# Performance work log

Hardware: AMD Instinct MI355X
Metric: run time of the kernel (lower is better)

Reference implementation:

```python
import jax, jax.numpy as jnp
import numpy as np

B, N, IN_F, OUT_F, H, NUM_EDGE_TYPES = 16, 512, 256, 256, 8, 50
HEAD_DIM = OUT_F // H
LN_EPS = 1e-5


def setup_inputs() -> dict:
    key = jax.random.key(0)
    ks = jax.random.split(key, 8)
    x = jax.random.normal(ks[0], (B, N, IN_F), dtype=jnp.float32)
    adj = jax.random.randint(ks[1], (B, N, N), 0, 2, dtype=jnp.int32)
    edge_types = jax.random.randint(ks[2], (B, N, N), 0, NUM_EDGE_TYPES, dtype=jnp.int32)
    # Parameters (torch Linear stores weight as [out, in]; we keep [in, out] for x @ W)
    W = jax.random.normal(ks[3], (IN_F, OUT_F), dtype=jnp.float32) / np.sqrt(IN_F)
    a1 = jax.random.normal(ks[4], (HEAD_DIM,), dtype=jnp.float32) / np.sqrt(HEAD_DIM)
    a2 = jax.random.normal(ks[5], (HEAD_DIM,), dtype=jnp.float32) / np.sqrt(HEAD_DIM)
    edge_emb = jax.random.normal(ks[6], (NUM_EDGE_TYPES, H), dtype=jnp.float32) * 0.02
    edge_emb = edge_emb.at[0].set(0.0)  # padding_idx=0
    ln_gamma = jnp.ones((OUT_F,), dtype=jnp.float32)
    ln_beta = jnp.zeros((OUT_F,), dtype=jnp.float32)
    return {"x": x, "adj": adj, "edge_types": edge_types, "W": W, "a1": a1,
            "a2": a2, "edge_emb": edge_emb, "ln_gamma": ln_gamma, "ln_beta": ln_beta}


def reference(x, adj, edge_types, W, a1, a2, edge_emb, ln_gamma, ln_beta):
    Bx, Nx, _ = x.shape
    # Wh: [B, N, H, D]
    Wh = (x @ W).reshape(Bx, Nx, H, HEAD_DIM)
    # per-node attention scalars: [B, N, H]
    s1 = jnp.einsum('bnhd,d->bnh', Wh, a1)
    s2 = jnp.einsum('bnhd,d->bnh', Wh, a2)
    # e: [B, N(i), N(j), H]
    e = s1[:, :, None, :] + s2[:, None, :, :] + edge_emb[edge_types]
    e = jnp.where(e > 0, e, 0.2 * e)  # leaky_relu(0.2)
    e = jnp.where((adj == 0)[..., None], jnp.float32(-1e9), e)
    alpha = jax.nn.softmax(e, axis=2)  # softmax over j
    # (dropout omitted: eval mode / deterministic reference)
    h = jnp.einsum('bijh,bjhd->bihd', alpha, Wh).reshape(Bx, Nx, OUT_F)
    # LayerNorm over last dim
    mu = jnp.mean(h, axis=-1, keepdims=True)
    var = jnp.mean(jnp.square(h - mu), axis=-1, keepdims=True)
    hn = (h - mu) * jax.lax.rsqrt(var + LN_EPS) * ln_gamma + ln_beta
    return jax.nn.elu(hn)
```

## Files before the change

### kernel.cpp

```cpp
#include <hip/hip_runtime.h>
#include <hip/hip_bf16.h>
#include <stdint.h>

namespace gat {
constexpr int NB   = 16;
constexpr int NN   = 512;
constexpr int FIN  = 256;
constexpr int FOUT = 256;
constexpr int H    = 8;
constexpr int NE   = 50;
constexpr float L2E  = 1.4426950408889634f;
constexpr float MASK = -115.41500f;
}
using namespace gat;

typedef __attribute__((ext_vector_type(8))) short short8;
typedef __attribute__((ext_vector_type(4))) float f32x4;

__device__ __forceinline__ unsigned pk_bf16(unsigned ulo, unsigned uhi) {
  return __builtin_amdgcn_perm(uhi, ulo, 0x07060302u);
}
__device__ __forceinline__ unsigned pk2f(float a, float b) {
  return pk_bf16(__float_as_uint(a) + 0x8000u, __float_as_uint(b) + 0x8000u);
}

__global__ __launch_bounds__(256) void k_prep(const float* __restrict__ Wm,
                                              unsigned short* __restrict__ WbT) {
  const int k  = threadIdx.x;
  const int f0 = blockIdx.x * 4;
  #pragma unroll
  for (int r = 0; r < 4; ++r) {
    const unsigned u = __float_as_uint(Wm[k * FOUT + f0 + r]) + 0x8000u;
    WbT[(f0 + r) * FIN + k] = (unsigned short)(u >> 16);
  }
}

__global__ __launch_bounds__(256, 4) void k_gemm(
    const float* __restrict__ x, const unsigned short* __restrict__ WbT,
    const float* __restrict__ a1, const float* __restrict__ a2,
    unsigned short* __restrict__ WhT, float* __restrict__ s1, float* __restrict__ s2T)
{
  __shared__ alignas(16) unsigned short xS[16 * 264];
  const int t    = threadIdx.x;
  const int row0 = blockIdx.x * 16;

  {
    const int r  = t >> 4;
    const int kb = (t & 15) * 16;
    const float4* xg = (const float4*)(x + (size_t)(row0 + r) * FIN + kb);
    const float4 v0 = xg[0], v1 = xg[1], v2 = xg[2], v3 = xg[3];
    uint4 o0, o1;
    o0.x = pk2f(v0.x, v0.y); o0.y = pk2f(v0.z, v0.w);
    o0.z = pk2f(v1.x, v1.y); o0.w = pk2f(v1.z, v1.w);
    o1.x = pk2f(v2.x, v2.y); o1.y = pk2f(v2.z, v2.w);
    o1.z = pk2f(v3.x, v3.y); o1.w = pk2f(v3.z, v3.w);
    *(uint4*)&xS[r * 264 + kb]     = o0;
    *(uint4*)&xS[r * 264 + kb + 8] = o1;
  }
  __syncthreads();

  const int w    = t >> 6;
  const int L    = t & 63;
  const int nn   = L & 15;
  const int quad = L >> 4;
  const unsigned short* wb = WbT + (size_t)(w * 64 + nn) * FIN + quad * 8;
  const unsigned short* xp = &xS[nn * 264 + quad * 8];

  f32x4 acc0 = {0.f,0.f,0.f,0.f}, acc1 = {0.f,0.f,0.f,0.f};
  f32x4 acc2 = {0.f,0.f,0.f,0.f}, acc3 = {0.f,0.f,0.f,0.f};

  #pragma unroll 2
  for (int kc = 0; kc < 8; ++kc) {
    const int k0 = kc * 32;
    const short8 A  = *(const short8*)(xp + k0);
    const short8 B0 = *(const short8*)(wb + k0);
    const short8 B1 = *(const short8*)(wb + 16 * FIN + k0);
    const short8 B2 = *(const short8*)(wb + 32 * FIN + k0);
    const short8 B3 = *(const short8*)(wb + 48 * FIN + k0);
    acc0 = __builtin_amdgcn_mfma_f32_16x16x32_bf16(A, B0, acc0, 0, 0, 0);
    acc1 = __builtin_amdgcn_mfma_f32_16x16x32_bf16(A, B1, acc1, 0, 0, 0);
    acc2 = __builtin_amdgcn_mfma_f32_16x16x32_bf16(A, B2, acc2, 0, 0, 0);
    acc3 = __builtin_amdgcn_mfma_f32_16x16x32_bf16(A, B3, acc3, 0, 0, 0);
  }

  const int b     = row0 >> 9;
  const int node0 = (row0 & 511) + quad * 4;
  f32x4 accs[4] = {acc0, acc1, acc2, acc3};

  #pragma unroll
  for (int ft = 0; ft < 4; ++ft) {
    const int f = w * 64 + ft * 16 + nn;
    uint2 o;
    o.x = pk2f(accs[ft][0], accs[ft][1]);
    o.y = pk2f(accs[ft][2], accs[ft][3]);
    *(uint2*)(WhT + (size_t)((b * 8 + (f >> 5)) * 32 + (f & 31)) * 512 + node0) = o;
  }

  const float a1lo = a1[nn], a1hi = a1[16 + nn];
  const float a2lo = a2[nn], a2hi = a2[16 + nn];
  #pragma unroll
  for (int hh = 0; hh < 2; ++hh) {
    const int h = w * 2 + hh;
    const f32x4 e0 = accs[hh * 2], e1 = accs[hh * 2 + 1];
    float p1[4], p2[4];
    #pragma unroll
    for (int r = 0; r < 4; ++r) {
      p1[r] = e0[r] * a1lo + e1[r] * a1hi;
      p2[r] = e0[r] * a2lo + e1[r] * a2hi;
    }
    #pragma unroll
    for (int r = 0; r < 4; ++r) {
      p1[r] += __shfl_xor(p1[r], 1); p2[r] += __shfl_xor(p2[r], 1);
      p1[r] += __shfl_xor(p1[r], 2); p2[r] += __shfl_xor(p2[r], 2);
      p1[r] += __shfl_xor(p1[r], 4); p2[r] += __shfl_xor(p2[r], 4);
      p1[r] += __shfl_xor(p1[r], 8); p2[r] += __shfl_xor(p2[r], 8);
    }
    if (nn == 0) {
      float4 sv; sv.x = p2[0] * L2E; sv.y = p2[1] * L2E; sv.z = p2[2] * L2E; sv.w = p2[3] * L2E;
      *(float4*)(s2T + (size_t)(b * 8 + h) * 512 + node0) = sv;
      #pragma unroll
      for (int r = 0; r < 4; ++r)
        s1[(size_t)(row0 + quad * 4 + r) * H + h] = p1[r] * L2E;
    }
  }
}

__global__ __launch_bounds__(256, 2) void k_attn(
    const int* __restrict__ adj, const int* __restrict__ ety,
    const float* __restrict__ s1, const float* __restrict__ s2T,
    const unsigned short* __restrict__ WhT, const float* __restrict__ emb,
    const float* __restrict__ gam, const float* __restrict__ bet,
    float* __restrict__ out)
{
  __shared__ float2 embS[4 * 64];
  __shared__ float2 lnS[16 * 4];

  const int t    = threadIdx.x;
  const int b    = blockIdx.x >> 5;
  const int i0   = (blockIdx.x & 31) * 16;
  const int w    = t >> 6;
  const int L    = t & 63;
  const int i    = L & 15;
  const int quad = L >> 4;
  const int h0   = w, h1 = w + 4;

  {
    const int wp = t >> 6, e = t & 63;
    if (e < NE) {
      float2 v; v.x = emb[e * H + wp] * L2E; v.y = emb[e * H + wp + 4] * L2E;
      embS[t] = v;
    }
  }

  const int row = b * NN + i0 + i;
  const float si0 = s1[(size_t)row * H + h0];
  const float si1 = s1[(size_t)row * H + h1];
  const int adjBase = row * NN;
  const float* s2h0 = s2T + (size_t)(b * 8 + h0) * 512;
  const float* s2h1 = s2T + (size_t)(b * 8 + h1) * 512;
  const unsigned short* wt00 = WhT + (size_t)((b * 8 + h0) * 32 + i)      * 512;
  const unsigned short* wt01 = WhT + (size_t)((b * 8 + h0) * 32 + 16 + i) * 512;
  const unsigned short* wt10 = WhT + (size_t)((b * 8 + h1) * 32 + i)      * 512;
  const unsigned short* wt11 = WhT + (size_t)((b * 8 + h1) * 32 + 16 + i) * 512;

  f32x4 acc00 = {0.f,0.f,0.f,0.f}, acc01 = {0.f,0.f,0.f,0.f};
  f32x4 acc10 = {0.f,0.f,0.f,0.f}, acc11 = {0.f,0.f,0.f,0.f};
  float l0 = 0.f, l1 = 0.f;

  __syncthreads();

  #pragma unroll 2
  for (int kc = 0; kc < 16; ++kc) {
    const int ja = kc * 32 + quad * 8;
    const int4 av0 = *(const int4*)(adj + adjBase + ja);
    const int4 av1 = *(const int4*)(adj + adjBase + ja + 4);
    const int4 ev0 = *(const int4*)(ety + adjBase + ja);
    const int4 ev1 = *(const int4*)(ety + adjBase + ja + 4);
    const float4 sa0 = *(const float4*)(s2h0 + ja);
    const float4 sb0 = *(const float4*)(s2h0 + ja + 4);
    const float4 sa1 = *(const float4*)(s2h1 + ja);
    const float4 sb1 = *(const float4*)(s2h1 + ja + 4);
    const short8 A00 = *(const short8*)(wt00 + ja);
    const short8 A01 = *(const short8*)(wt01 + ja);
    const short8 A10 = *(const short8*)(wt10 + ja);
    const short8 A11 = *(const short8*)(wt11 + ja);

    const int aq[8] = {av0.x, av0.y, av0.z, av0.w, av1.x, av1.y, av1.z, av1.w};
    const int eq[8] = {ev0.x, ev0.y, ev0.z, ev0.w, ev1.x, ev1.y, ev1.z, ev1.w};
    const float s20[8] = {sa0.x, sa0.y, sa0.z, sa0.w, sb0.x, sb0.y, sb0.z, sb0.w};
    const float s21[8] = {sa1.x, sa1.y, sa1.z, sa1.w, sb1.x, sb1.y, sb1.z, sb1.w};

    unsigned u0[8], u1[8];
    #pragma unroll
    for (int q = 0; q < 8; ++q) {
      const float2 em = embS[w * 64 + eq[q]];
      const bool on = (aq[q] != 0);
      float e0 = si0 + s20[q] + em.x;
      float e1 = si1 + s21[q] + em.y;
      e0 = fmaxf(e0, 0.2f * e0);
      e1 = fmaxf(e1, 0.2f * e1);
      e0 = on ? e0 : MASK;
      e1 = on ? e1 : MASK;
      const float p0 = exp2f(e0);
      const float p1 = exp2f(e1);
      l0 += p0; l1 += p1;
      u0[q] = __float_as_uint(p0) + 0x8000u;
      u1[q] = __float_as_uint(p1) + 0x8000u;
    }
    uint4 U0, U1;
    U0.x = pk_bf16(u0[0], u0[1]); U0.y = pk_bf16(u0[2], u0[3]);
    U0.z = pk_bf16(u0[4], u0[5]); U0.w = pk_bf16(u0[6], u0[7]);
    U1.x = pk_bf16(u1[0], u1[1]); U1.y = pk_bf16(u1[2], u1[3]);
    U1.z = pk_bf16(u1[4], u1[5]); U1.w = pk_bf16(u1[6], u1[7]);
    const short8 B0 = __builtin_bit_cast(short8, U0);
    const short8 B1 = __builtin_bit_cast(short8, U1);

    acc00 = __builtin_amdgcn_mfma_f32_16x16x32_bf16(A00, B0, acc00, 0, 0, 0);
    acc01 = __builtin_amdgcn_mfma_f32_16x16x32_bf16(A01, B0, acc01, 0, 0, 0);
    acc10 = __builtin_amdgcn_mfma_f32_16x16x32_bf16(A10, B1, acc10, 0, 0, 0);
    acc11 = __builtin_amdgcn_mfma_f32_16x16x32_bf16(A11, B1, acc11, 0, 0, 0);
  }

  l0 += __shfl_xor(l0, 16); l0 += __shfl_xor(l0, 32);
  l1 += __shfl_xor(l1, 16); l1 += __shfl_xor(l1, 32);
  const float inv0 = __builtin_amdgcn_rcpf(l0);
  const float inv1 = __builtin_amdgcn_rcpf(l1);

  float vals[16];
  #pragma unroll
  for (int r = 0; r < 4; ++r) {
    vals[r]      = acc00[r] * inv0;
    vals[4 + r]  = acc01[r] * inv0;
    vals[8 + r]  = acc10[r] * inv1;
    vals[12 + r] = acc11[r] * inv1;
  }

  float s = 0.f, ss = 0.f;
  #pragma unroll
  for (int k = 0; k < 16; ++k) { s += vals[k]; ss += vals[k] * vals[k]; }
  s += __shfl_xor(s, 16); ss += __shfl_xor(ss, 16);
  s += __shfl_xor(s, 32); ss += __shfl_xor(ss, 32);
  if (quad == 0) { float2 v; v.x = s; v.y = ss; lnS[i * 4 + w] = v; }
  __syncthreads();
  float S = 0.f, SS = 0.f;
  #pragma unroll
  for (int ww = 0; ww < 4; ++ww) { const float2 v = lnS[i * 4 + ww]; S += v.x; SS += v.y; }
  const float mu   = S * (1.0f / 256.0f);
  const float var  = SS * (1.0f / 256.0f) - mu * mu;
  const float rstd = rsqrtf(var + 1e-5f);

  const int fb[4] = { h0 * 32 + quad * 4, h0 * 32 + 16 + quad * 4,
                      h1 * 32 + quad * 4, h1 * 32 + 16 + quad * 4 };
  #pragma unroll
  for (int g = 0; g < 4; ++g) {
    const float4 gv = *(const float4*)(gam + fb[g]);
    const float4 bv = *(const float4*)(bet + fb[g]);
    float4 o;
    o.x = (vals[g*4+0] - mu) * rstd * gv.x + bv.x;
    o.y = (vals[g*4+1] - mu) * rstd * gv.y + bv.y;
    o.z = (vals[g*4+2] - mu) * rstd * gv.z + bv.z;
    o.w = (vals[g*4+3] - mu) * rstd * gv.w + bv.w;
    o.x = o.x > 0.f ? o.x : exp2f(o.x * L2E) - 1.f;
    o.y = o.y > 0.f ? o.y : exp2f(o.y * L2E) - 1.f;
    o.z = o.z > 0.f ? o.z : exp2f(o.z * L2E) - 1.f;
    o.w = o.w > 0.f ? o.w : exp2f(o.w * L2E) - 1.f;
    *(float4*)(out + (size_t)row * FOUT + fb[g]) = o;
  }
}

extern "C" void kernel_launch(void* const* d_in, const int* in_sizes, int n_in,
                              void* d_out, int out_size, void* d_ws, size_t ws_size,
                              hipStream_t stream) {
  (void)in_sizes; (void)n_in; (void)out_size; (void)ws_size;
  const float* x   = (const float*)d_in[0];
  const int*   adj = (const int*)  d_in[1];
  const int*   ety = (const int*)  d_in[2];
  const float* Wm  = (const float*)d_in[3];
  const float* a1  = (const float*)d_in[4];
  const float* a2  = (const float*)d_in[5];
  const float* emb = (const float*)d_in[6];
  const float* gam = (const float*)d_in[7];
  const float* bet = (const float*)d_in[8];
  float* out = (float*)d_out;

  unsigned short* WhT = (unsigned short*)d_ws;
  unsigned short* WbT = WhT + (size_t)NB * H * 32 * 512;
  float* s1  = (float*)(WbT + (size_t)FOUT * FIN);
  float* s2T = s1 + (size_t)NB * NN * H;

  k_prep<<<dim3(64),  dim3(256), 0, stream>>>(Wm, WbT);
  k_gemm<<<dim3(NB * NN / 16), dim3(256), 0, stream>>>(x, WbT, a1, a2, WhT, s1, s2T);
  k_attn<<<dim3(NB * (NN / 16)), dim3(256), 0, stream>>>(adj, ety, s1, s2T, WhT, emb, gam, bet, out);
}
```

Baseline: 141.5 us.

## Split K/J reduction across two wave groups with LDS combine in gemm and attention

Both the projection GEMM and the attention kernel now launch 512-thread blocks. The reduction dimension is split in half between two groups of four waves, and the upper half's partial accumulators (plus softmax denominators) are combined through shared memory. The weight-transpose prep kernel is also reshaped to one thread per element with coalesced reads. The aim is more waves in flight to hide the memory latency of the adj and edge-type streams. The cost is extra LDS traffic, an added barrier, and half the waves sitting idle during the epilogue. There is also a leftover redundant store loop in the gemm reduction.

```diff
diff --git a/kernel.cpp b/kernel.cpp
--- a/kernel.cpp
+++ b/kernel.cpp
@@ -26,51 +26,48 @@
 
 __global__ __launch_bounds__(256) void k_prep(const float* __restrict__ Wm,
                                               unsigned short* __restrict__ WbT) {
-  const int k  = threadIdx.x;
-  const int f0 = blockIdx.x * 4;
-  #pragma unroll
-  for (int r = 0; r < 4; ++r) {
-    const unsigned u = __float_as_uint(Wm[k * FOUT + f0 + r]) + 0x8000u;
-    WbT[(f0 + r) * FIN + k] = (unsigned short)(u >> 16);
-  }
-}
-
-__global__ __launch_bounds__(256, 4) void k_gemm(
+  const int k = blockIdx.x;
+  const int f = threadIdx.x;
+  const unsigned u = __float_as_uint(Wm[k * FOUT + f]) + 0x8000u;
+  WbT[f * FIN + k] = (unsigned short)(u >> 16);
+}
+
+__global__ __launch_bounds__(512, 4) void k_gemm(
     const float* __restrict__ x, const unsigned short* __restrict__ WbT,
     const float* __restrict__ a1, const float* __restrict__ a2,
     unsigned short* __restrict__ WhT, float* __restrict__ s1, float* __restrict__ s2T)
 {
   __shared__ alignas(16) unsigned short xS[16 * 264];
+  __shared__ float redG[256 * 18];
   const int t    = threadIdx.x;
   const int row0 = blockIdx.x * 16;
 
   {
-    const int r  = t >> 4;
-    const int kb = (t & 15) * 16;
+    const int r  = t >> 5;
+    const int kb = (t & 31) * 8;
     const float4* xg = (const float4*)(x + (size_t)(row0 + r) * FIN + kb);
-    const float4 v0 = xg[0], v1 = xg[1], v2 = xg[2], v3 = xg[3];
-    uint4 o0, o1;
-    o0.x = pk2f(v0.x, v0.y); o0.y = pk2f(v0.z, v0.w);
-    o0.z = pk2f(v1.x, v1.y); o0.w = pk2f(v1.z, v1.w);
-    o1.x = pk2f(v2.x, v2.y); o1.y = pk2f(v2.z, v2.w);
-    o1.z = pk2f(v3.x, v3.y); o1.w = pk2f(v3.z, v3.w);
-    *(uint4*)&xS[r * 264 + kb]     = o0;
-    *(uint4*)&xS[r * 264 + kb + 8] = o1;
-  }
-  __syncthreads();
-
-  const int w    = t >> 6;
+    const float4 v0 = xg[0], v1 = xg[1];
+    uint4 o;
+    o.x = pk2f(v0.x, v0.y); o.y = pk2f(v0.z, v0.w);
+    o.z = pk2f(v1.x, v1.y); o.w = pk2f(v1.z, v1.w);
+    *(uint4*)&xS[r * 264 + kb] = o;
+  }
+  __syncthreads();
+
+  const int W    = t >> 6;
+  const int w    = W & 3;
+  const int kh   = W >> 2;
   const int L    = t & 63;
   const int nn   = L & 15;
   const int quad = L >> 4;
-  const unsigned short* wb = WbT + (size_t)(w * 64 + nn) * FIN + quad * 8;
-  const unsigned short* xp = &xS[nn * 264 + quad * 8];
+  const unsigned short* wb = WbT + (size_t)(w * 64 + nn) * FIN + kh * 128 + quad * 8;
+  const unsigned short* xp = &xS[nn * 264 + kh * 128 + quad * 8];
 
   f32x4 acc0 = {0.f,0.f,0.f,0.f}, acc1 = {0.f,0.f,0.f,0.f};
   f32x4 acc2 = {0.f,0.f,0.f,0.f}, acc3 = {0.f,0.f,0.f,0.f};
 
-  #pragma unroll 2
-  for (int kc = 0; kc < 8; ++kc) {
+  #pragma unroll
+  for (int kc = 0; kc < 4; ++kc) {
     const int k0 = kc * 32;
     const short8 A  = *(const short8*)(xp + k0);
     const short8 B0 = *(const short8*)(wb + k0);
@@ -83,6 +80,29 @@
     acc3 = __builtin_amdgcn_mfma_f32_16x16x32_bf16(A, B3, acc3, 0, 0, 0);
   }
 
+  const int tt = (w << 6) | L;
+  if (kh == 1) {
+    float* rp = redG + tt * 18;
+    #pragma unroll
+    for (int r = 0; r < 4; ++r) {
+      ((float2*)rp)[r]     = {acc0[r * 2 & 3], 0.f};
+    }
+    rp[0]=acc0[0]; rp[1]=acc0[1]; rp[2]=acc0[2]; rp[3]=acc0[3];
+    rp[4]=acc1[0]; rp[5]=acc1[1]; rp[6]=acc1[2]; rp[7]=acc1[3];
+    rp[8]=acc2[0]; rp[9]=acc2[1]; rp[10]=acc2[2]; rp[11]=acc2[3];
+    rp[12]=acc3[0]; rp[13]=acc3[1]; rp[14]=acc3[2]; rp[15]=acc3[3];
+  }
+  __syncthreads();
+  if (kh == 1) return;
+
+  {
+    const float* rp = redG + tt * 18;
+    acc0[0]+=rp[0]; acc0[1]+=rp[1]; acc0[2]+=rp[2]; acc0[3]+=rp[3];
+    acc1[0]+=rp[4]; acc1[1]+=rp[5]; acc1[2]+=rp[6]; acc1[3]+=rp[7];
+    acc2[0]+=rp[8]; acc2[1]+=rp[9]; acc2[2]+=rp[10]; acc2[3]+=rp[11];
+    acc3[0]+=rp[12]; acc3[1]+=rp[13]; acc3[2]+=rp[14]; acc3[3]+=rp[15];
+  }
+
   const int b     = row0 >> 9;
   const int node0 = (row0 & 511) + quad * 4;
   f32x4 accs[4] = {acc0, acc1, acc2, acc3};
@@ -125,7 +145,7 @@
   }
 }
 
-__global__ __launch_bounds__(256, 2) void k_attn(
+__global__ __launch_bounds__(512, 4) void k_attn(
     const int* __restrict__ adj, const int* __restrict__ ety,
     const float* __restrict__ s1, const float* __restrict__ s2T,
     const unsigned short* __restrict__ WhT, const float* __restrict__ emb,
@@ -134,17 +154,20 @@
 {
   __shared__ float2 embS[4 * 64];
   __shared__ float2 lnS[16 * 4];
+  __shared__ float  redS[256 * 18];
 
   const int t    = threadIdx.x;
   const int b    = blockIdx.x >> 5;
   const int i0   = (blockIdx.x & 31) * 16;
-  const int w    = t >> 6;
+  const int W    = t >> 6;
+  const int w    = W & 3;
+  const int jh   = W >> 2;
   const int L    = t & 63;
   const int i    = L & 15;
   const int quad = L >> 4;
   const int h0   = w, h1 = w + 4;
 
-  {
+  if (t < 256) {
     const int wp = t >> 6, e = t & 63;
     if (e < NE) {
       float2 v; v.x = emb[e * H + wp] * L2E; v.y = emb[e * H + wp + 4] * L2E;
@@ -156,6 +179,7 @@
   const float si0 = s1[(size_t)row * H + h0];
   const float si1 = s1[(size_t)row * H + h1];
   const int adjBase = row * NN;
+  const int jbase   = jh * 256;
   const float* s2h0 = s2T + (size_t)(b * 8 + h0) * 512;
   const float* s2h1 = s2T + (size_t)(b * 8 + h1) * 512;
   const unsigned short* wt00 = WhT + (size_t)((b * 8 + h0) * 32 + i)      * 512;
@@ -170,8 +194,8 @@
   __syncthreads();
 
   #pragma unroll 2
-  for (int kc = 0; kc < 16; ++kc) {
-    const int ja = kc * 32 + quad * 8;
+  for (int kc = 0; kc < 8; ++kc) {
+    const int ja = jbase + kc * 32 + quad * 8;
     const int4 av0 = *(const int4*)(adj + adjBase + ja);
     const int4 av1 = *(const int4*)(adj + adjBase + ja + 4);
     const int4 ev0 = *(const int4*)(ety + adjBase + ja);
@@ -223,31 +247,53 @@
 
   l0 += __shfl_xor(l0, 16); l0 += __shfl_xor(l0, 32);
   l1 += __shfl_xor(l1, 16); l1 += __shfl_xor(l1, 32);
-  const float inv0 = __builtin_amdgcn_rcpf(l0);
-  const float inv1 = __builtin_amdgcn_rcpf(l1);
-
-  float vals[16];
-  #pragma unroll
-  for (int r = 0; r < 4; ++r) {
-    vals[r]      = acc00[r] * inv0;
-    vals[4 + r]  = acc01[r] * inv0;
-    vals[8 + r]  = acc10[r] * inv1;
-    vals[12 + r] = acc11[r] * inv1;
-  }
-
-  float s = 0.f, ss = 0.f;
-  #pragma unroll
-  for (int k = 0; k < 16; ++k) { s += vals[k]; ss += vals[k] * vals[k]; }
-  s += __shfl_xor(s, 16); ss += __shfl_xor(ss, 16);
-  s += __shfl_xor(s, 32); ss += __shfl_xor(ss, 32);
-  if (quad == 0) { float2 v; v.x = s; v.y = ss; lnS[i * 4 + w] = v; }
-  __syncthreads();
-  float S = 0.f, SS = 0.f;
-  #pragma unroll
-  for (int ww = 0; ww < 4; ++ww) { const float2 v = lnS[i * 4 + ww]; S += v.x; SS += v.y; }
-  const float mu   = S * (1.0f / 256.0f);
-  const float var  = SS * (1.0f / 256.0f) - mu * mu;
-  const float rstd = rsqrtf(var + 1e-5f);
+
+  const int tt = (w << 6) | L;
+  if (jh == 1) {
+    float* rp = redS + tt * 18;
+    rp[0]=acc00[0]; rp[1]=acc00[1]; rp[2]=acc00[2]; rp[3]=acc00[3];
+    rp[4]=acc01[0]; rp[5]=acc01[1]; rp[6]=acc01[2]; rp[7]=acc01[3];
+    rp[8]=acc10[0]; rp[9]=acc10[1]; rp[10]=acc10[2]; rp[11]=acc10[3];
+    rp[12]=acc11[0]; rp[13]=acc11[1]; rp[14]=acc11[2]; rp[15]=acc11[3];
+    rp[16]=l0; rp[17]=l1;
+  }
+  __syncthreads();
+
+  float vals[16]; float mu, rstd;
+  if (jh == 0) {
+    const float* rp = redS + tt * 18;
+    acc00[0]+=rp[0]; acc00[1]+=rp[1]; acc00[2]+=rp[2]; acc00[3]+=rp[3];
+    acc01[0]+=rp[4]; acc01[1]+=rp[5]; acc01[2]+=rp[6]; acc01[3]+=rp[7];
+    acc10[0]+=rp[8]; acc10[1]+=rp[9]; acc10[2]+=rp[10]; acc10[3]+=rp[11];
+    acc11[0]+=rp[12]; acc11[1]+=rp[13]; acc11[2]+=rp[14]; acc11[3]+=rp[15];
+    l0 += rp[16]; l1 += rp[17];
+    const float inv0 = __builtin_amdgcn_rcpf(l0);
+    const float inv1 = __builtin_amdgcn_rcpf(l1);
+    #pragma unroll
+    for (int r = 0; r < 4; ++r) {
+      vals[r]      = acc00[r] * inv0;
+      vals[4 + r]  = acc01[r] * inv0;
+      vals[8 + r]  = acc10[r] * inv1;
+      vals[12 + r] = acc11[r] * inv1;
+    }
+    float s = 0.f, ss = 0.f;
+    #pragma unroll
+    for (int k = 0; k < 16; ++k) { s += vals[k]; ss += vals[k] * vals[k]; }
+    s += __shfl_xor(s, 16); ss += __shfl_xor(ss, 16);
+    s += __shfl_xor(s, 32); ss += __shfl_xor(ss, 32);
+    if (quad == 0) { float2 v; v.x = s; v.y = ss; lnS[i * 4 + w] = v; }
+  }
+  __syncthreads();
+  if (jh == 1) return;
+
+  {
+    float S = 0.f, SS = 0.f;
+    #pragma unroll
+    for (int ww = 0; ww < 4; ++ww) { const float2 v = lnS[i * 4 + ww]; S += v.x; SS += v.y; }
+    mu = S * (1.0f / 256.0f);
+    const float var = SS * (1.0f / 256.0f) - mu * mu;
+    rstd = rsqrtf(var + 1e-5f);
+  }
 
   const int fb[4] = { h0 * 32 + quad * 4, h0 * 32 + 16 + quad * 4,
                       h1 * 32 + quad * 4, h1 * 32 + 16 + quad * 4 };
@@ -288,7 +334,7 @@
   float* s1  = (float*)(WbT + (size_t)FOUT * FIN);
   float* s2T = s1 + (size_t)NB * NN * H;
 
-  k_prep<<<dim3(64),  dim3(256), 0, stream>>>(Wm, WbT);
-  k_gemm<<<dim3(NB * NN / 16), dim3(256), 0, stream>>>(x, WbT, a1, a2, WhT, s1, s2T);
-  k_attn<<<dim3(NB * (NN / 16)), dim3(256), 0, stream>>>(adj, ety, s1, s2T, WhT, emb, gam, bet, out);
-}
+  k_prep<<<dim3(FIN),  dim3(256), 0, stream>>>(Wm, WbT);
+  k_gemm<<<dim3(NB * NN / 16), dim3(512), 0, stream>>>(x, WbT, a1, a2, WhT, s1, s2T);
+  k_attn<<<dim3(NB * (NN / 16)), dim3(512), 0, stream>>>(adj, ety, s1, s2T, WhT, emb, gam, bet, out);
+}
```

Measured after the change: 139.4 us. No clear change (-1.5%).
